# Kernel tuning notes

Measured on AMD Instinct MI355X. Metric: run time of the kernel, lower is better.

The kernel has to match this reference:

```python
import jax, jax.numpy as jnp
import numpy as np

S, B, F, H, L, T = 256, 64, 256, 768, 3, 32  # seq_len, batch, features, hidden, layers, target_len


def setup_inputs() -> dict:
    key = jax.random.key(0)
    ks = jax.random.split(key, 16)
    s = 1.0 / np.sqrt(H)  # PyTorch LSTM/Linear uniform init bound
    u = lambda k, shape: jax.random.uniform(k, shape, jnp.float32, -s, s)
    return {
        "x": jax.random.normal(ks[0], (S, B, F), jnp.float32),
        # encoder layer 0: input_size -> hidden_size
        "e_Wih0": u(ks[1], (4 * H, F)), "e_Whh0": u(ks[2], (4 * H, H)),
        "e_bih0": u(ks[3], (4 * H,)), "e_bhh0": u(ks[4], (4 * H,)),
        # encoder layers 1..L-1 (stacked): hidden -> hidden
        "e_Wih": u(ks[5], (L - 1, 4 * H, H)), "e_Whh": u(ks[6], (L - 1, 4 * H, H)),
        "e_bih": u(ks[7], (L - 1, 4 * H)), "e_bhh": u(ks[8], (L - 1, 4 * H)),
        # decoder layers (stacked): hidden -> hidden
        "d_Wih": u(ks[9], (L, 4 * H, H)), "d_Whh": u(ks[10], (L, 4 * H, H)),
        "d_bih": u(ks[11], (L, 4 * H)), "d_bhh": u(ks[12], (L, 4 * H)),
        # output head: hidden -> input_size
        "lin_W": u(ks[13], (F, H)), "lin_b": u(ks[14], (F,)),
        "target_len": T,
    }


def _cell(gates, c_prev):
    # PyTorch gate order: input, forget, cell(g), output
    i, f, g, o = jnp.split(gates, 4, axis=-1)
    c = jax.nn.sigmoid(f) * c_prev + jax.nn.sigmoid(i) * jnp.tanh(g)
    h = jax.nn.sigmoid(o) * jnp.tanh(c)
    return h, c


def reference(x, e_Wih0, e_Whh0, e_bih0, e_bhh0, e_Wih, e_Whh, e_bih, e_bhh,
              d_Wih, d_Whh, d_bih, d_bhh, lin_W, lin_b, target_len):
    Bb = x.shape[1]
    Hh = e_Whh0.shape[1]
    dt = x.dtype

    # --- encoder layer 0: full-sequence LSTM from zero state ---
    b0 = e_bih0 + e_bhh0
    def enc_step(carry, x_t):
        h, c = carry
        h, c = _cell(x_t @ e_Wih0.T + h @ e_Whh0.T + b0, c)
        return (h, c), None
    z = jnp.zeros((Bb, Hh), dt)
    (h, _), _ = jax.lax.scan(enc_step, (z, z), x)

    # --- encoder layers 1..L-1: each sees previous layer's final hidden as a
    # seq_len=1 input with fresh zero (h0, c0) -> W_hh term vanishes ---
    enc = [h]
    xin = h
    for l in range(e_Wih.shape[0]):
        hl, _ = _cell(xin @ e_Wih[l].T + (e_bih[l] + e_bhh[l]), 0.0)
        enc.append(hl)
        xin = hl
    encoder_hidden = jnp.stack(enc)  # (L, B, H)

    # --- decoder: recursive. Call-site bug passes zeros as initial hidden_list.
    # Each step, each layer i independently runs a 1-step LSTM on its own previous
    # hidden with fresh zero state (W_hh unused, cell not carried). Only the last
    # layer's hidden feeds the Linear head. ---
    d_b = (d_bih + d_bhh)[:, None, :]  # (L, 1, 4H)
    def dec_step(hs, _):
        gates = jnp.einsum('lbh,lgh->lbg', hs, d_Wih) + d_b
        hn, _ = _cell(gates, 0.0)
        out_t = hn[-1] @ lin_W.T + lin_b  # (B, F)
        return hn, out_t
    h0 = jnp.zeros((d_Wih.shape[0], Bb, Hh), dt)
    _, outputs = jax.lax.scan(dec_step, h0, None, length=target_len)  # (T, B, F)

    return outputs, encoder_hidden
```

## Files before the change

kernel.cpp:

```cpp
#include <hip/hip_runtime.h>
#include <hip/hip_bf16.h>


constexpr int NB = 64;
constexpr int NH = 768;
constexpr int NF = 256;
constexpr int NS = 256;
constexpr int NT = 32;
constexpr int ENC_BLOCKS = 96;
constexpr int ENC_GROUP  = 48;
constexpr int DEC_BLOCKS = 48;

typedef short bf16x8 __attribute__((ext_vector_type(8)));
typedef float f32x4 __attribute__((ext_vector_type(4)));

__device__ __forceinline__ float sigm(float x) { return 1.f / (1.f + expf(-x)); }

__device__ __forceinline__ int4 ld_i4_cohere(const int4* p) {
    int4 v;
    asm volatile("global_load_dwordx4 %0, %1, off sc0 sc1" : "=v"(v) : "v"(p));
    return v;
}
__device__ __forceinline__ int ld_i1_cohere_sync(const int* p) {
    int v;
    asm volatile("global_load_dword %0, %1, off sc0 sc1\n\ts_waitcnt vmcnt(0)"
                 : "=v"(v) : "v"(p) : "memory");
    return v;
}
__device__ __forceinline__ void st_i1_cohere(int* p, int v) {
    asm volatile("global_store_dword %0, %1, off sc0 sc1" :: "v"(p), "v"(v) : "memory");
}
__device__ __forceinline__ void vm_drain() {
    asm volatile("s_waitcnt vmcnt(0)" ::: "memory");
}

__device__ __forceinline__ void arrive(int* slots, int idx, int phase) {
    if (threadIdx.x == 0) st_i1_cohere(slots + idx * 16, phase);
}
__device__ __forceinline__ void wait_all(int* slots, int phase, int nb) {
    if (threadIdx.x < nb) {
        const int* p = slots + threadIdx.x * 16;
        while (ld_i1_cohere_sync(p) < phase) __builtin_amdgcn_s_sleep(1);
    }
    __syncthreads();
}

__global__ __launch_bounds__(256) void cvt_all(
    const float* __restrict__ s0,
    const float* __restrict__ s1,
    const float* __restrict__ s2,
    const float* __restrict__ s3,
    __hip_bfloat16* __restrict__ d)
{
    const int i = (blockIdx.x * 256 + threadIdx.x) * 4;
    const float* s; int off;
    if (i < 4194304)      { s = s0; off = 0; }
    else if (i < 4980736) { s = s1; off = 4194304; }
    else if (i < 7340032) { s = s2; off = 4980736; }
    else                  { s = s3; off = 7340032; }
    const float4 v = *(const float4*)(s + (i - off));
    d[i]     = __float2bfloat16(v.x);
    d[i + 1] = __float2bfloat16(v.y);
    d[i + 2] = __float2bfloat16(v.z);
    d[i + 3] = __float2bfloat16(v.w);
}

__global__ __launch_bounds__(256, 1) void enc_persist(
    const __hip_bfloat16* __restrict__ xb,
    const __hip_bfloat16* __restrict__ Wx,
    const __hip_bfloat16* __restrict__ Wh,
    const float* __restrict__ bih, const float* __restrict__ bhh,
    int* __restrict__ h0buf,
    int* __restrict__ h1buf,
    float* __restrict__ enc0,
    int* slots)
{
    const int bu = blockIdx.x % (NH / 16);
    const int bm = blockIdx.x / (NH / 16);
    int* gslots = slots + bm * ENC_GROUP * 16;
    const int u0 = bu * 16;
    const int tid = threadIdx.x;
    const int g = tid >> 6;
    const int lane = tid & 63;
    const int r = lane & 15;
    const int q = lane >> 4;
    const int row0 = bm * 32 + r;
    const int row1 = row0 + 16;

    const size_t wrow = (size_t)(g * NH + u0 + r);
    bf16x8 wx[8], wh[24];
    #pragma unroll
    for (int c = 0; c < 8; ++c)
        wx[c] = *(const bf16x8*)(Wx + wrow * NF + c * 32 + q * 8);
    #pragma unroll
    for (int c = 0; c < 24; ++c)
        wh[c] = *(const bf16x8*)(Wh + wrow * NH + c * 32 + q * 8);

    __shared__ int   hst[32 * 388];
    __shared__ float gbuf[4][32][17];
    __shared__ float lbias[64];
    if (tid < 64)
        lbias[tid] = bih[(tid >> 4) * NH + u0 + (tid & 15)]
                   + bhh[(tid >> 4) * NH + u0 + (tid & 15)];
    __syncthreads();

    float cst[2] = {0.f, 0.f};

    for (int t = 0; t < NS; ++t) {
        const int* hcur = (t & 1) ? h1buf : h0buf;
        int* hnext      = (t & 1) ? h0buf : h1buf;
        const __hip_bfloat16* xt = xb + (size_t)t * NB * NF;

        f32x4 acc0 = {0.f, 0.f, 0.f, 0.f};
        f32x4 acc1 = {0.f, 0.f, 0.f, 0.f};
        #pragma unroll
        for (int c = 0; c < 8; ++c) {
            const bf16x8 a0 = *(const bf16x8*)(xt + (size_t)row0 * NF + c * 32 + q * 8);
            const bf16x8 a1 = *(const bf16x8*)(xt + (size_t)row1 * NF + c * 32 + q * 8);
            acc0 = __builtin_amdgcn_mfma_f32_16x16x32_bf16(a0, wx[c], acc0, 0, 0, 0);
            acc1 = __builtin_amdgcn_mfma_f32_16x16x32_bf16(a1, wx[c], acc1, 0, 0, 0);
        }

        if (t > 0) wait_all(gslots, t, ENC_GROUP);

        {
            const int4* src = (const int4*)hcur + bm * 3072;
            int4 v[12];
            #pragma unroll
            for (int i = 0; i < 12; ++i) v[i] = ld_i4_cohere(src + i * 256 + tid);
            vm_drain();
            #pragma unroll
            for (int i = 0; i < 12; ++i) {
                const int k = i * 256 + tid;
                const int rw = k / 96, cl = k % 96;
                *(int4*)(hst + rw * 388 + cl * 4) = v[i];
            }
        }
        __syncthreads();

        #pragma unroll
        for (int c = 0; c < 24; ++c) {
            const bf16x8 a0 = *(const bf16x8*)((const short*)hst + r * 776 + c * 32 + q * 8);
            const bf16x8 a1 = *(const bf16x8*)((const short*)hst + (r + 16) * 776 + c * 32 + q * 8);
            acc0 = __builtin_amdgcn_mfma_f32_16x16x32_bf16(a0, wh[c], acc0, 0, 0, 0);
            acc1 = __builtin_amdgcn_mfma_f32_16x16x32_bf16(a1, wh[c], acc1, 0, 0, 0);
        }

        #pragma unroll
        for (int i = 0; i < 4; ++i) {
            gbuf[g][q * 4 + i][r]      = acc0[i];
            gbuf[g][16 + q * 4 + i][r] = acc1[i];
        }
        __syncthreads();

        {
            const int rowl = tid >> 3, pair = tid & 7;
            const int ua = pair * 2;
            float h2[2];
            #pragma unroll
            for (int e = 0; e < 2; ++e) {
                const int ul = ua + e;
                const float pi = gbuf[0][rowl][ul] + lbias[ul];
                const float pf = gbuf[1][rowl][ul] + lbias[16 + ul];
                const float pg = gbuf[2][rowl][ul] + lbias[32 + ul];
                const float po = gbuf[3][rowl][ul] + lbias[48 + ul];
                const float cn = sigm(pf) * cst[e] + sigm(pi) * tanhf(pg);
                h2[e] = sigm(po) * tanhf(cn);
                cst[e] = cn;
            }
            const int b = bm * 32 + rowl;
            if (t == NS - 1) {
                enc0[(size_t)b * NH + u0 + ua]     = h2[0];
                enc0[(size_t)b * NH + u0 + ua + 1] = h2[1];
                __hip_bfloat16* hf = (__hip_bfloat16*)hnext;
                hf[(size_t)b * NH + u0 + ua]     = __float2bfloat16(h2[0]);
                hf[(size_t)b * NH + u0 + ua + 1] = __float2bfloat16(h2[1]);
            } else {
                union { __hip_bfloat16 b16; unsigned short s; } c0, c1;
                c0.b16 = __float2bfloat16(h2[0]);
                c1.b16 = __float2bfloat16(h2[1]);
                const int pv = (int)c0.s | ((int)c1.s << 16);
                st_i1_cohere(hnext + (size_t)b * 384 + (u0 >> 1) + pair, pv);
            }
        }
        if (t < NS - 1) {
            vm_drain();
            __syncthreads();
            arrive(gslots, bu, t + 1);
        }
    }
}

template<int KX, int KH>
__global__ __launch_bounds__(256) void lstm_step(
    const __hip_bfloat16* __restrict__ xin,
    const __hip_bfloat16* __restrict__ hin,
    const __hip_bfloat16* __restrict__ Wx,
    const __hip_bfloat16* __restrict__ Wh,
    const float* __restrict__ bih, const float* __restrict__ bhh,
    const float* __restrict__ c_in,
    __hip_bfloat16* __restrict__ h_bf,
    float* __restrict__ h_f32,
    float* __restrict__ c_out)
{
    constexpr int K = KX + KH;
    constexpr int NCH = K / 32;
    const int bu = blockIdx.x % (NH / 16);
    const int bm = blockIdx.x / (NH / 16);
    const int u0 = bu * 16;
    const int tid = threadIdx.x;
    const int g = tid >> 6;
    const int lane = tid & 63;
    const int r = lane & 15;
    const int q = lane >> 4;

    f32x4 acc0 = {0.f, 0.f, 0.f, 0.f};
    f32x4 acc1 = {0.f, 0.f, 0.f, 0.f};
    const int row0 = bm * 32 + r;
    const int row1 = row0 + 16;
    const long wr = (long)(g * NH + u0 + r);

    #pragma unroll
    for (int c = 0; c < NCH; ++c) {
        const int k0 = c * 32;
        bf16x8 a0, a1, bfrag;
        if (k0 < KX) {
            const int kk = k0 + q * 8;
            a0 = *(const bf16x8*)(xin + (long)row0 * KX + kk);
            a1 = *(const bf16x8*)(xin + (long)row1 * KX + kk);
            bfrag = *(const bf16x8*)(Wx + wr * KX + kk);
        } else {
            const int kk = (k0 - KX) + q * 8;
            a0 = *(const bf16x8*)(hin + (long)row0 * KH + kk);
            a1 = *(const bf16x8*)(hin + (long)row1 * KH + kk);
            bfrag = *(const bf16x8*)(Wh + wr * KH + kk);
        }
        acc0 = __builtin_amdgcn_mfma_f32_16x16x32_bf16(a0, bfrag, acc0, 0, 0, 0);
        acc1 = __builtin_amdgcn_mfma_f32_16x16x32_bf16(a1, bfrag, acc1, 0, 0, 0);
    }

    __shared__ float gbuf[4][32][17];
    #pragma unroll
    for (int i = 0; i < 4; ++i) {
        gbuf[g][q * 4 + i][r]      = acc0[i];
        gbuf[g][16 + q * 4 + i][r] = acc1[i];
    }
    __syncthreads();

    #pragma unroll
    for (int i = 0; i < 2; ++i) {
        const int idx = tid + i * 256;
        const int bl = idx >> 4;
        const int u  = idx & 15;
        const int gu = u0 + u;
        const int b  = bm * 32 + bl;
        const float pi = gbuf[0][bl][u] + bih[gu]          + bhh[gu];
        const float pf = gbuf[1][bl][u] + bih[NH + gu]     + bhh[NH + gu];
        const float pg = gbuf[2][bl][u] + bih[2 * NH + gu] + bhh[2 * NH + gu];
        const float po = gbuf[3][bl][u] + bih[3 * NH + gu] + bhh[3 * NH + gu];
        const float cp = c_in ? c_in[(long)b * NH + gu] : 0.f;
        const float cn = sigm(pf) * cp + sigm(pi) * tanhf(pg);
        const float hn = sigm(po) * tanhf(cn);
        if (c_out) c_out[(long)b * NH + gu] = cn;
        if (h_f32) h_f32[(long)b * NH + gu] = hn;
        h_bf[(long)b * NH + gu] = __float2bfloat16(hn);
    }
}

__global__ __launch_bounds__(256) void dec_persist(
    const float* __restrict__ W,
    const float* __restrict__ bih, const float* __restrict__ bhh,
    float* __restrict__ hd0, float* __restrict__ hd1,
    float* __restrict__ hall, int* slots)
{
    __shared__ float hstD[768];
    const int tid = threadIdx.x;
    const int ul = tid >> 4;
    const int j  = tid & 15;
    const int u  = blockIdx.x * 16 + ul;
    const float* Wi = W + (size_t)u * NH;
    const float* Wg = W + (size_t)(2 * NH + u) * NH;
    const float* Wo = W + (size_t)(3 * NH + u) * NH;
    const float bi = bih[u]          + bhh[u];
    const float bg = bih[2 * NH + u] + bhh[2 * NH + u];
    const float bo = bih[3 * NH + u] + bhh[3 * NH + u];

    for (int t = 0; t < NT; ++t) {
        const float* hin = (t & 1) ? hd1 : hd0;
        float* hout      = (t & 1) ? hd0 : hd1;
        if (t > 0) wait_all(slots, t, DEC_BLOCKS);
        if (tid < 192) {
            int4 v = ld_i4_cohere((const int4*)hin + tid);
            vm_drain();
            ((int4*)hstD)[tid] = v;
        }
        __syncthreads();
        float ai = 0.f, ag = 0.f, ao = 0.f;
        for (int k = j; k < NH; k += 16) {
            const float hv = hstD[k];
            ai += hv * Wi[k];
            ag += hv * Wg[k];
            ao += hv * Wo[k];
        }
        #pragma unroll
        for (int off = 8; off > 0; off >>= 1) {
            ai += __shfl_xor(ai, off, 16);
            ag += __shfl_xor(ag, off, 16);
            ao += __shfl_xor(ao, off, 16);
        }
        if (j == 0) {
            const float cn = sigm(ai + bi) * tanhf(ag + bg);
            const float hn = sigm(ao + bo) * tanhf(cn);
            hall[(size_t)t * NH + u] = hn;
            if (t < NT - 1)
                st_i1_cohere((int*)(hout + u), __float_as_int(hn));
        }
        if (t < NT - 1) {
            vm_drain();
            __syncthreads();
            arrive(slots, blockIdx.x, t + 1);
        }
    }
}

__global__ __launch_bounds__(256) void head_kernel(
    const float* __restrict__ hall,
    const float* __restrict__ lw,
    const float* __restrict__ lb,
    float* __restrict__ out)
{
    const int t = blockIdx.x;
    const int f = threadIdx.x;
    const float* h = hall + (size_t)t * NH;
    const float4* wrow = (const float4*)(lw + (size_t)f * NH);
    float acc = 0.f;
    for (int k4 = 0; k4 < NH / 4; ++k4) {
        const float4 w = wrow[k4];
        acc += h[k4 * 4]     * w.x;
        acc += h[k4 * 4 + 1] * w.y;
        acc += h[k4 * 4 + 2] * w.z;
        acc += h[k4 * 4 + 3] * w.w;
    }
    acc += lb[f];
    float* o = out + (size_t)t * NB * NF + f;
    for (int b = 0; b < NB; ++b) o[(size_t)b * NF] = acc;
}

extern "C" void kernel_launch(void* const* d_in, const int* in_sizes, int n_in,
                              void* d_out, int out_size, void* d_ws, size_t ws_size,
                              hipStream_t stream) {
    (void)in_sizes; (void)n_in; (void)out_size; (void)ws_size;
    const float* x     = (const float*)d_in[0];
    const float* eWih0 = (const float*)d_in[1];
    const float* eWhh0 = (const float*)d_in[2];
    const float* ebih0 = (const float*)d_in[3];
    const float* ebhh0 = (const float*)d_in[4];
    const float* eWih  = (const float*)d_in[5];
    const float* ebih  = (const float*)d_in[7];
    const float* ebhh  = (const float*)d_in[8];
    const float* dWih  = (const float*)d_in[9];
    const float* dbih  = (const float*)d_in[11];
    const float* dbhh  = (const float*)d_in[12];
    const float* linW  = (const float*)d_in[13];
    const float* linb  = (const float*)d_in[14];
    float* out = (float*)d_out;

    char* ws = (char*)d_ws;
    __hip_bfloat16* xb   = (__hip_bfloat16*)(ws);
    __hip_bfloat16* W0x  = (__hip_bfloat16*)(ws +  8388608);
    __hip_bfloat16* W0h  = (__hip_bfloat16*)(ws +  9961472);
    __hip_bfloat16* eW12 = (__hip_bfloat16*)(ws + 14680064);
    int* hbi0 = (int*)(ws + 24117248);
    int* hbi1 = (int*)(ws + 24215552);
    float* hd0  = (float*)(ws + 24313856);
    float* hd1  = (float*)(ws + 24316928);
    float* hall = (float*)(ws + 24320000);
    int* bar    = (int*)(ws + 24418304);
    int* enc_slots = bar;
    int* dec_slots = bar + 2048;

    (void)hipMemsetAsync(hbi0, 0, (size_t)NB * NH * 2, stream);
    (void)hipMemsetAsync(hd0, 0, (size_t)NH * 4, stream);
    (void)hipMemsetAsync(bar, 0, 16384, stream);

    cvt_all<<<12058624 / 1024, 256, 0, stream>>>(x, eWih0, eWhh0, eWih,
                                                 (__hip_bfloat16*)ws);

    float* enc = out + (size_t)NT * NB * NF;

    enc_persist<<<ENC_BLOCKS, 256, 0, stream>>>(
        xb, W0x, W0h, ebih0, ebhh0, hbi0, hbi1, enc, enc_slots);

    __hip_bfloat16* hb0 = (__hip_bfloat16*)hbi0;
    __hip_bfloat16* hb1 = (__hip_bfloat16*)hbi1;
    lstm_step<NH, 0><<<96, 256, 0, stream>>>(
        hb0, nullptr, eW12, nullptr, ebih, ebhh,
        nullptr, hb1, enc + NB * NH, nullptr);
    lstm_step<NH, 0><<<96, 256, 0, stream>>>(
        hb1, nullptr, eW12 + (size_t)4 * NH * NH, nullptr,
        ebih + 4 * NH, ebhh + 4 * NH,
        nullptr, hb0, enc + 2 * (size_t)NB * NH, nullptr);

    const float* W2 = dWih + (size_t)2 * 4 * NH * NH;
    dec_persist<<<DEC_BLOCKS, 256, 0, stream>>>(
        W2, dbih + 2 * 4 * NH, dbhh + 2 * 4 * NH, hd0, hd1, hall, dec_slots);

    head_kernel<<<NT, NF, 0, stream>>>(hall, linW, linb, out);
}
```

Baseline: 1.800 ms.

## Run decoder recurrence concurrently with encoder in one persistent launch

The decoder chain does not depend on the encoder, because it starts from zero hidden state. It is moved into extra blocks of the encoder's persistent kernel so the two recurrences run side by side instead of back to back. This removes the decoder's serialized runtime and one kernel launch. The trade-offs are a larger grid, which must still be fully co-resident for the spin barriers to avoid deadlock, and extra shared memory declared for every block.

```diff
diff --git a/kernel.cpp b/kernel.cpp
--- a/kernel.cpp
+++ b/kernel.cpp
@@ -65,7 +65,7 @@
     d[i + 3] = __float2bfloat16(v.w);
 }
 
-__global__ __launch_bounds__(256, 1) void enc_persist(
+__global__ __launch_bounds__(256, 1) void enc_dec_persist(
     const __hip_bfloat16* __restrict__ xb,
     const __hip_bfloat16* __restrict__ Wx,
     const __hip_bfloat16* __restrict__ Wh,
@@ -73,13 +73,74 @@
     int* __restrict__ h0buf,
     int* __restrict__ h1buf,
     float* __restrict__ enc0,
-    int* slots)
+    int* slots,
+    const float* __restrict__ dW,
+    const float* __restrict__ dbih, const float* __restrict__ dbhh,
+    float* __restrict__ hd0, float* __restrict__ hd1,
+    float* __restrict__ hall, int* dslots)
 {
+    __shared__ int   hst[32 * 388];
+    __shared__ float gbuf[4][32][17];
+    __shared__ float lbias[64];
+    __shared__ float hstD[768];
+
+    const int tid = threadIdx.x;
+
+    if (blockIdx.x >= ENC_BLOCKS) {
+        const int dbid = blockIdx.x - ENC_BLOCKS;
+        const int ul = tid >> 4;
+        const int j  = tid & 15;
+        const int u  = dbid * 16 + ul;
+        const float* Wi = dW + (size_t)u * NH;
+        const float* Wg = dW + (size_t)(2 * NH + u) * NH;
+        const float* Wo = dW + (size_t)(3 * NH + u) * NH;
+        const float bi = dbih[u]          + dbhh[u];
+        const float bg = dbih[2 * NH + u] + dbhh[2 * NH + u];
+        const float bo = dbih[3 * NH + u] + dbhh[3 * NH + u];
+
+        for (int t = 0; t < NT; ++t) {
+            const float* hin = (t & 1) ? hd1 : hd0;
+            float* hout      = (t & 1) ? hd0 : hd1;
+            if (t > 0) wait_all(dslots, t, DEC_BLOCKS);
+            if (tid < 192) {
+                int4 v = ld_i4_cohere((const int4*)hin + tid);
+                vm_drain();
+                ((int4*)hstD)[tid] = v;
+            }
+            __syncthreads();
+            float ai = 0.f, ag = 0.f, ao = 0.f;
+            for (int k = j; k < NH; k += 16) {
+                const float hv = hstD[k];
+                ai += hv * Wi[k];
+                ag += hv * Wg[k];
+                ao += hv * Wo[k];
+            }
+            #pragma unroll
+            for (int off = 8; off > 0; off >>= 1) {
+                ai += __shfl_xor(ai, off, 16);
+                ag += __shfl_xor(ag, off, 16);
+                ao += __shfl_xor(ao, off, 16);
+            }
+            if (j == 0) {
+                const float cn = sigm(ai + bi) * tanhf(ag + bg);
+                const float hn = sigm(ao + bo) * tanhf(cn);
+                hall[(size_t)t * NH + u] = hn;
+                if (t < NT - 1)
+                    st_i1_cohere((int*)(hout + u), __float_as_int(hn));
+            }
+            if (t < NT - 1) {
+                vm_drain();
+                __syncthreads();
+                arrive(dslots, dbid, t + 1);
+            }
+        }
+        return;
+    }
+
     const int bu = blockIdx.x % (NH / 16);
     const int bm = blockIdx.x / (NH / 16);
     int* gslots = slots + bm * ENC_GROUP * 16;
     const int u0 = bu * 16;
-    const int tid = threadIdx.x;
     const int g = tid >> 6;
     const int lane = tid & 63;
     const int r = lane & 15;
@@ -96,9 +157,6 @@
     for (int c = 0; c < 24; ++c)
         wh[c] = *(const bf16x8*)(Wh + wrow * NH + c * 32 + q * 8);
 
-    __shared__ int   hst[32 * 388];
-    __shared__ float gbuf[4][32][17];
-    __shared__ float lbias[64];
     if (tid < 64)
         lbias[tid] = bih[(tid >> 4) * NH + u0 + (tid & 15)]
                    + bhh[(tid >> 4) * NH + u0 + (tid & 15)];
@@ -267,62 +325,6 @@
     }
 }
 
-__global__ __launch_bounds__(256) void dec_persist(
-    const float* __restrict__ W,
-    const float* __restrict__ bih, const float* __restrict__ bhh,
-    float* __restrict__ hd0, float* __restrict__ hd1,
-    float* __restrict__ hall, int* slots)
-{
-    __shared__ float hstD[768];
-    const int tid = threadIdx.x;
-    const int ul = tid >> 4;
-    const int j  = tid & 15;
-    const int u  = blockIdx.x * 16 + ul;
-    const float* Wi = W + (size_t)u * NH;
-    const float* Wg = W + (size_t)(2 * NH + u) * NH;
-    const float* Wo = W + (size_t)(3 * NH + u) * NH;
-    const float bi = bih[u]          + bhh[u];
-    const float bg = bih[2 * NH + u] + bhh[2 * NH + u];
-    const float bo = bih[3 * NH + u] + bhh[3 * NH + u];
-
-    for (int t = 0; t < NT; ++t) {
-        const float* hin = (t & 1) ? hd1 : hd0;
-        float* hout      = (t & 1) ? hd0 : hd1;
-        if (t > 0) wait_all(slots, t, DEC_BLOCKS);
-        if (tid < 192) {
-            int4 v = ld_i4_cohere((const int4*)hin + tid);
-            vm_drain();
-            ((int4*)hstD)[tid] = v;
-        }
-        __syncthreads();
-        float ai = 0.f, ag = 0.f, ao = 0.f;
-        for (int k = j; k < NH; k += 16) {
-            const float hv = hstD[k];
-            ai += hv * Wi[k];
-            ag += hv * Wg[k];
-            ao += hv * Wo[k];
-        }
-        #pragma unroll
-        for (int off = 8; off > 0; off >>= 1) {
-            ai += __shfl_xor(ai, off, 16);
-            ag += __shfl_xor(ag, off, 16);
-            ao += __shfl_xor(ao, off, 16);
-        }
-        if (j == 0) {
-            const float cn = sigm(ai + bi) * tanhf(ag + bg);
-            const float hn = sigm(ao + bo) * tanhf(cn);
-            hall[(size_t)t * NH + u] = hn;
-            if (t < NT - 1)
-                st_i1_cohere((int*)(hout + u), __float_as_int(hn));
-        }
-        if (t < NT - 1) {
-            vm_drain();
-            __syncthreads();
-            arrive(slots, blockIdx.x, t + 1);
-        }
-    }
-}
-
 __global__ __launch_bounds__(256) void head_kernel(
     const float* __restrict__ hall,
     const float* __restrict__ lw,
@@ -388,8 +390,10 @@
 
     float* enc = out + (size_t)NT * NB * NF;
 
-    enc_persist<<<ENC_BLOCKS, 256, 0, stream>>>(
-        xb, W0x, W0h, ebih0, ebhh0, hbi0, hbi1, enc, enc_slots);
+    const float* W2 = dWih + (size_t)2 * 4 * NH * NH;
+    enc_dec_persist<<<ENC_BLOCKS + DEC_BLOCKS, 256, 0, stream>>>(
+        xb, W0x, W0h, ebih0, ebhh0, hbi0, hbi1, enc, enc_slots,
+        W2, dbih + 2 * 4 * NH, dbhh + 2 * 4 * NH, hd0, hd1, hall, dec_slots);
 
     __hip_bfloat16* hb0 = (__hip_bfloat16*)hbi0;
     __hip_bfloat16* hb1 = (__hip_bfloat16*)hbi1;
@@ -401,9 +405,5 @@
         ebih + 4 * NH, ebhh + 4 * NH,
         nullptr, hb0, enc + 2 * (size_t)NB * NH, nullptr);
 
-    const float* W2 = dWih + (size_t)2 * 4 * NH * NH;
-    dec_persist<<<DEC_BLOCKS, 256, 0, stream>>>(
-        W2, dbih + 2 * 4 * NH, dbhh + 2 * 4 * NH, hd0, hd1, hall, dec_slots);
-
     head_kernel<<<NT, NF, 0, stream>>>(hall, linW, linb, out);
 }
```

Result: faster. 1.561 ms (-13.3%).
